# Performance work log

Measured on AMD Instinct MI355X. Metric: run time of the kernel, lower is better.

## Reference

```python
import jax, jax.numpy as jnp
import numpy as np

B, M, K, P = 64, 8, 4, 16  # batch, rx antennas, streams, constellation size
NBPS = 4  # 16-QAM


def _qam_points(nbps):
    # square QAM, unit average energy
    n = 2 ** (nbps // 2)
    pam = 2.0 * np.arange(n) - n + 1.0  # e.g. {-3,-1,1,3}
    re, im = np.meshgrid(pam, pam, indexing='ij')
    pts = (re + 1j * im).reshape(-1)
    pts = pts / np.sqrt(np.mean(np.abs(pts) ** 2))
    return pts.astype(np.complex64)


def _build_vecs(points, k):
    # replicate MaximumLikelihoodDetector._build_vecs: stream 0 varies slowest
    p = points.shape[0]
    grids = np.meshgrid(*([np.arange(p)] * k), indexing='ij')
    idx = np.stack(grids, axis=-1).reshape(-1, k)        # [P^K, K]
    vecs = points[idx]                                   # [P^K, K] complex
    c = np.stack([
        np.stack([np.where(idx[:, j] == pi)[0] for j in range(k)], axis=-1)
        for pi in range(p)
    ], axis=-1)                                          # [P^(K-1), K, P]
    return vecs, c.astype(np.int32)


def setup_inputs() -> dict:
    key = jax.random.key(0)
    ks = jax.random.split(key, 6)
    points = _qam_points(NBPS)
    vecs, c = _build_vecs(points, K)
    yr = jax.random.normal(ks[0], (B, M), jnp.float32)
    yi = jax.random.normal(ks[1], (B, M), jnp.float32)
    hr = jax.random.normal(ks[2], (B, M, K), jnp.float32)
    hi = jax.random.normal(ks[3], (B, M, K), jnp.float32)
    # Hermitian positive-definite noise covariance s = A A^H / M + I
    ar = jax.random.normal(ks[4], (B, M, M), jnp.float32)
    ai = jax.random.normal(ks[5], (B, M, M), jnp.float32)
    a = (ar + 1j * ai).astype(jnp.complex64)
    s = a @ jnp.conj(jnp.swapaxes(a, -1, -2)) / M + jnp.eye(M, dtype=jnp.complex64)
    return {
        'yr': yr, 'yi': yi, 'hr': hr, 'hi': hi,
        'sr': jnp.real(s).astype(jnp.float32), 'si': jnp.imag(s).astype(jnp.float32),
        'vr': jnp.asarray(vecs.real), 'vi': jnp.asarray(vecs.imag),
        'c': jnp.asarray(c),
    }


def reference(yr, yi, hr, hi, sr, si, vr, vi, c):
    y = (yr + 1j * yi).astype(jnp.complex64)          # [B, M]
    h = (hr + 1j * hi).astype(jnp.complex64)          # [B, M, K]
    s = (sr + 1j * si).astype(jnp.complex64)          # [B, M, M]
    vecs = (vr + 1j * vi).astype(jnp.complex64)       # [V, K]
    # whitening: s_inv = inv(cholesky(s))
    L = jnp.linalg.cholesky(s)
    s_inv = jnp.linalg.inv(L)                         # [B, M, M]
    yw = jnp.einsum('bmn,bn->bm', s_inv, y)           # [B, M]
    hw = jnp.einsum('bmn,bnk->bmk', s_inv, h)         # [B, M, K]
    # distances for every candidate symbol vector
    hv = jnp.einsum('bmk,vk->bvm', hw, vecs)          # [B, V, M]
    diff = yw[:, None, :] - hv                        # [B, V, M]
    exponents = -jnp.sum(diff.real ** 2 + diff.imag ** 2, axis=-1)  # [B, V]
    # regroup exponents by (stream, symbol) and reduce (app -> logsumexp)
    exp_g = exponents[:, c]                           # [B, P^(K-1), K, P]
    logits = jax.nn.logsumexp(exp_g, axis=-3)         # [B, K, P]
    return logits
```

## Files before the change

### kernel.cpp

```cpp
#include <hip/hip_runtime.h>
#include <math.h>


__global__ __launch_bounds__(256) void k_main(
    const float* __restrict__ yr, const float* __restrict__ yi,
    const float* __restrict__ hr, const float* __restrict__ hi,
    const float* __restrict__ sr, const float* __restrict__ si,
    const float* __restrict__ vr, const float* __restrict__ vi,
    float* __restrict__ ws, float* __restrict__ out)
{
    __shared__ float sL[8][8][2];
    __shared__ float sDinv[8];
    __shared__ float lyw[8][2];
    __shared__ float lhw[8][4][2];
    __shared__ float tab[4][8][16][2];
    __shared__ float pn2b[16];
    __shared__ float Hn1b;
    __shared__ float xbuf[16][256];
    __shared__ float pmax[256];
    __shared__ float cm[16][17];
    __shared__ float m1buf[16], m2buf[16], m3buf[16];
    __shared__ float part2[256], part3[256];
    __shared__ float s2buf[16];

    const int t = threadIdx.x;
    const int b = blockIdx.x >> 4, chunk = blockIdx.x & 15;
    const int lane = t & 63, wv = t >> 6;
    const int i3 = t & 15, i2 = t >> 4;

    if (wv == 0) {
        float ar_[8] = {}, ai_[8] = {}, Lr_[8] = {}, Li_[8] = {};
        if (lane < 8) {
#pragma unroll
            for (int k = 0; k < 8; ++k) {
                ar_[k] = sr[b * 64 + lane * 8 + k];
                ai_[k] = si[b * 64 + lane * 8 + k];
            }
        }
        float inv = 0.f;
#pragma unroll
        for (int j = 0; j < 8; ++j) {
            if (lane == j) {
                float d = ar_[j];
#pragma unroll
                for (int k = 0; k < 8; ++k) if (k < j) d -= Lr_[k]*Lr_[k] + Li_[k]*Li_[k];
                float ld = sqrtf(d);
                Lr_[j] = ld; Li_[j] = 0.f;
                inv = 1.f / ld;
                sDinv[j] = inv;
            }
            float invj = __shfl(inv, j);
            float cr = ar_[j], ci = ai_[j];
#pragma unroll
            for (int k = 0; k < 8; ++k) if (k < j) {
                float Ljrk = __shfl(Lr_[k], j);
                float Ljik = __shfl(Li_[k], j);
                cr -= Lr_[k]*Ljrk + Li_[k]*Ljik;
                ci -= Li_[k]*Ljrk - Lr_[k]*Ljik;
            }
            if (lane < 8 && lane > j) { Lr_[j] = cr * invj; Li_[j] = ci * invj; }
        }
        if (lane < 8) {
#pragma unroll
            for (int k = 0; k < 8; ++k) if (k <= lane) { sL[lane][k][0] = Lr_[k]; sL[lane][k][1] = Li_[k]; }
        }
        if (lane < 5) {
            float rr[8], ri[8], zr[8], zi[8];
            if (lane == 0) {
#pragma unroll
                for (int i = 0; i < 8; ++i) { rr[i] = yr[b*8+i]; ri[i] = yi[b*8+i]; }
            } else {
#pragma unroll
                for (int i = 0; i < 8; ++i) { rr[i] = hr[(b*8+i)*4 + (lane-1)]; ri[i] = hi[(b*8+i)*4 + (lane-1)]; }
            }
#pragma unroll
            for (int i = 0; i < 8; ++i) {
                float cr = rr[i], ci = ri[i];
#pragma unroll
                for (int k = 0; k < 8; ++k) if (k < i) {
                    cr -= sL[i][k][0]*zr[k] - sL[i][k][1]*zi[k];
                    ci -= sL[i][k][0]*zi[k] + sL[i][k][1]*zr[k];
                }
                float dv = sDinv[i];
                zr[i] = cr * dv; zi[i] = ci * dv;
                if (lane == 0) { lyw[i][0] = zr[i]; lyw[i][1] = zi[i]; }
                else           { lhw[i][lane-1][0] = zr[i]; lhw[i][lane-1][1] = zi[i]; }
            }
        }
        {
            int p = lane & 15;
            float pr  = vr[(p << 12) * 4];
            float pim = vi[(p << 12) * 4];
            if (lane < 16) pn2b[lane] = pr*pr + pim*pim;
            if (lane == 0) {
                float hn = 0.f;
#pragma unroll
                for (int m = 0; m < 8; ++m) hn += lhw[m][1][0]*lhw[m][1][0] + lhw[m][1][1]*lhw[m][1][1];
                Hn1b = hn;
            }
#pragma unroll
            for (int it = 0; it < 8; ++it) {
                int e = lane + it * 64;
                int k = e >> 7, m = (e >> 4) & 7;
                float hre = lhw[m][k][0], him = lhw[m][k][1];
                tab[k][m][p][0] = hre*pr  - him*pim;
                tab[k][m][p][1] = hre*pim + him*pr;
            }
        }
    }
    __syncthreads();

    float br_[8], bi_[8];
    float B2 = 0.f;
#pragma unroll
    for (int m = 0; m < 8; ++m) {
        const float2 t0 = *(const float2*)&tab[0][m][chunk][0];
        const float2 t2 = *(const float2*)&tab[2][m][i2][0];
        const float2 t3 = *(const float2*)&tab[3][m][i3][0];
        const float2 yw = *(const float2*)&lyw[m][0];
        br_[m] = t0.x + t2.x + t3.x - yw.x;
        bi_[m] = t0.y + t2.y + t3.y - yw.y;
        B2 = fmaf(br_[m], br_[m], fmaf(bi_[m], bi_[m], B2));
    }
    const float Hn1 = Hn1b;

    float x_[16];
    float vmA = -3.4e38f;
#pragma unroll
    for (int s = 0; s < 16; ++s) {
        float D = 0.f;
#pragma unroll
        for (int m = 0; m < 8; ++m) {
            const float2 t1 = *(const float2*)&tab[1][m][s][0];
            D = fmaf(br_[m], t1.x, D);
            D = fmaf(bi_[m], t1.y, D);
        }
        float x = fmaf(-2.f, D, -fmaf(pn2b[s], Hn1, B2));
        x_[s] = x;
        vmA = fmaxf(vmA, x);
        xbuf[s][t] = x;
    }
    pmax[t] = vmA;
    __syncthreads();

    const int su = i3, seg = i2;
    {
        float m = -3.4e38f;
#pragma unroll
        for (int j = 0; j < 16; ++j) m = fmaxf(m, xbuf[su][seg*16 + ((j + su) & 15)]);
        cm[su][seg] = m;
    }
    if (t < 16) {
        float m = -3.4e38f;
#pragma unroll
        for (int j = 0; j < 16; ++j) m = fmaxf(m, pmax[t*16 + j]);
        m2buf[t] = m;
    } else if (t < 32) {
        int d = t - 16;
        float m = -3.4e38f;
#pragma unroll
        for (int j = 0; j < 16; ++j) m = fmaxf(m, pmax[d + 16*j]);
        m3buf[d] = m;
    }
    __syncthreads();

    if (t < 16) {
        float m = -3.4e38f;
#pragma unroll
        for (int j = 0; j < 16; ++j) m = fmaxf(m, cm[t][j]);
        m1buf[t] = m;
    }
    const float M2 = m2buf[i2], M3 = m3buf[i3];
    const float Mlo = fminf(M2, M3);
    float acc = 0.f;
#pragma unroll
    for (int s = 0; s < 16; ++s) acc += __expf(x_[s] - Mlo);
    part2[t] = acc * __expf(Mlo - M2);
    part3[t] = acc * __expf(Mlo - M3);
    __syncthreads();

    {
        const float M1 = m1buf[su];
        float ssum = 0.f;
#pragma unroll
        for (int j = 0; j < 16; ++j)
            ssum += __expf(xbuf[su][seg*16 + ((j + su) & 15)] - M1);
        cm[su][seg] = ssum;
    }
    if (t < 16) {
        float S2 = 0.f;
#pragma unroll
        for (int j = 0; j < 16; ++j) S2 += part2[t*16 + j];
        s2buf[t] = S2;
        float* w = ws + ((b*48 + 16 + t)*16 + chunk)*2;
        w[0] = m2buf[t]; w[1] = S2;
    } else if (t < 32) {
        int d = t - 16;
        float S3 = 0.f;
#pragma unroll
        for (int j = 0; j < 16; ++j) S3 += part3[d + 16*j];
        float* w = ws + ((b*48 + 32 + d)*16 + chunk)*2;
        w[0] = m3buf[d]; w[1] = S3;
    }
    __syncthreads();

    if (t < 16) {
        float S1 = 0.f;
#pragma unroll
        for (int j = 0; j < 16; ++j) S1 += cm[t][j];
        float* w = ws + ((b*48 + t)*16 + chunk)*2;
        w[0] = m1buf[t]; w[1] = S1;
    }
    if (t == 16) {
        float M0 = m2buf[0];
#pragma unroll
        for (int i = 1; i < 16; ++i) M0 = fmaxf(M0, m2buf[i]);
        float S0 = 0.f;
#pragma unroll
        for (int i = 0; i < 16; ++i) S0 += s2buf[i] * __expf(m2buf[i] - M0);
        out[b*64 + chunk] = __logf(S0) + M0;
    }
}

__global__ __launch_bounds__(256) void k_comb(const float* __restrict__ ws, float* __restrict__ out)
{
    int idx = blockIdx.x * 256 + threadIdx.x;
    if (idx >= 64 * 48) return;
    int b = idx / 48, gi = idx % 48;
    const float* p = ws + (b*48 + gi)*32;
    float M = p[0];
#pragma unroll
    for (int i = 1; i < 16; ++i) M = fmaxf(M, p[2*i]);
    float S = 0.f;
#pragma unroll
    for (int i = 0; i < 16; ++i) S += p[2*i+1] * __expf(p[2*i] - M);
    out[b*64 + 16 + gi] = __logf(S) + M;
}

extern "C" void kernel_launch(void* const* d_in, const int* in_sizes, int n_in,
                              void* d_out, int out_size, void* d_ws, size_t ws_size,
                              hipStream_t stream) {
    const float* yr = (const float*)d_in[0];
    const float* yi = (const float*)d_in[1];
    const float* hr = (const float*)d_in[2];
    const float* hi = (const float*)d_in[3];
    const float* sr = (const float*)d_in[4];
    const float* si = (const float*)d_in[5];
    const float* vr = (const float*)d_in[6];
    const float* vi = (const float*)d_in[7];
    float* ws = (float*)d_ws;
    float* out = (float*)d_out;
    hipLaunchKernelGGL(k_main, dim3(1024), dim3(256), 0, stream,
                       yr, yi, hr, hi, sr, si, vr, vi, ws, out);
    hipLaunchKernelGGL(k_comb, dim3(12), dim3(256), 0, stream, ws, out);
}
```

Before: 19.71 us.

## Fuse into one per-batch kernel using Gram-matrix expansion of distances

Replaces the two-kernel design (1024 blocks plus a combine kernel) with one 1024-thread block per batch element that loops over 16 chunks and combines the logsumexp pairs in shared memory. Distances are expanded algebraically into precomputed Gram terms (per-stream norms, pairwise cross terms, projections onto yw), so each candidate costs a few table adds instead of an 8-element complex dot product. It also switches to exp2/log2 hardware builtins with pre-scaled constants and staggers the shared-memory reduction reads. This removes the second launch and the workspace round trip, at the cost of far fewer blocks (64) and more block-wide barriers per block.

```diff
diff --git a/kernel.cpp b/kernel.cpp
--- a/kernel.cpp
+++ b/kernel.cpp
@@ -1,34 +1,55 @@
 #include <hip/hip_runtime.h>
 #include <math.h>
 
-
-__global__ __launch_bounds__(256) void k_main(
+#define LOG2E 1.4426950408889634f
+#define LN2   0.6931471805599453f
+
+#if __has_builtin(__builtin_amdgcn_exp2f)
+#define EXP2(x) __builtin_amdgcn_exp2f(x)
+#else
+#define EXP2(x) exp2f(x)
+#endif
+#if __has_builtin(__builtin_amdgcn_logf)
+#define LOG2(x) __builtin_amdgcn_logf(x)
+#else
+#define LOG2(x) log2f(x)
+#endif
+
+
+__global__ __launch_bounds__(1024) void k_all(
     const float* __restrict__ yr, const float* __restrict__ yi,
     const float* __restrict__ hr, const float* __restrict__ hi,
     const float* __restrict__ sr, const float* __restrict__ si,
     const float* __restrict__ vr, const float* __restrict__ vi,
-    float* __restrict__ ws, float* __restrict__ out)
+    float* __restrict__ out)
 {
     __shared__ float sL[8][8][2];
     __shared__ float sDinv[8];
     __shared__ float lyw[8][2];
     __shared__ float lhw[8][4][2];
-    __shared__ float tab[4][8][16][2];
-    __shared__ float pn2b[16];
-    __shared__ float Hn1b;
-    __shared__ float xbuf[16][256];
-    __shared__ float pmax[256];
-    __shared__ float cm[16][17];
-    __shared__ float m1buf[16], m2buf[16], m3buf[16];
-    __shared__ float part2[256], part3[256];
-    __shared__ float s2buf[16];
+    __shared__ float ptr_[16], pti_[16];
+    __shared__ float gdiag[4];
+    __shared__ float gr2[6], gi2[6];
+    __shared__ float wr_[4], wi_[4];
+    __shared__ float u2s;
+    __shared__ float G2[4][16];
+    __shared__ float P2[6][16][16];
+    __shared__ float xbuf[4][16][256];
+    __shared__ float pmax[4][256];
+    __shared__ float cm[4][16][17];
+    __shared__ float m1b[4][16], m2b[4][16], m3b[4][16], s2b[4][16];
+    __shared__ float part2[4][256], part3[4][256];
+    __shared__ float pairs[48][17][2];
 
     const int t = threadIdx.x;
-    const int b = blockIdx.x >> 4, chunk = blockIdx.x & 15;
-    const int lane = t & 63, wv = t >> 6;
-    const int i3 = t & 15, i2 = t >> 4;
-
-    if (wv == 0) {
+    const int b = blockIdx.x;
+    const int u = t >> 8, c = t & 255;
+    const int i2 = c >> 4, i3 = c & 15;
+
+    if (t < 16) { ptr_[t] = vr[(t << 12) * 4]; pti_[t] = vi[(t << 12) * 4]; }
+
+    if (t < 64) {
+        const int lane = t;
         float ar_[8] = {}, ai_[8] = {}, Lr_[8] = {}, Li_[8] = {};
         if (lane < 8) {
 #pragma unroll
@@ -87,154 +108,175 @@
                 else           { lhw[i][lane-1][0] = zr[i]; lhw[i][lane-1][1] = zi[i]; }
             }
         }
+    }
+    __syncthreads();
+
+    if (t < 15) {
+        if (t < 4) {
+            float s = 0.f;
+#pragma unroll
+            for (int m = 0; m < 8; ++m) {
+                float ar = lhw[m][t][0], ai = lhw[m][t][1];
+                s = fmaf(ar, ar, fmaf(ai, ai, s));
+            }
+            gdiag[t] = s;
+        } else if (t < 10) {
+            const int pi = t - 4;
+            const int pa_tab[6] = {0, 0, 0, 1, 1, 2};
+            const int pb_tab[6] = {1, 2, 3, 2, 3, 3};
+            const int pa = pa_tab[pi];
+            const int pb = pb_tab[pi];
+            float srr = 0.f, sii = 0.f;
+#pragma unroll
+            for (int m = 0; m < 8; ++m) {
+                float ar = lhw[m][pa][0], ai = lhw[m][pa][1];
+                float br = lhw[m][pb][0], bi = lhw[m][pb][1];
+                srr = fmaf(ar, br, fmaf(ai, bi, srr));
+                sii = fmaf(ar, bi, fmaf(-ai, br, sii));
+            }
+            gr2[pi] = srr; gi2[pi] = sii;
+        } else if (t < 14) {
+            const int a = t - 10;
+            float swr = 0.f, swi = 0.f;
+#pragma unroll
+            for (int m = 0; m < 8; ++m) {
+                float ar = lhw[m][a][0], ai = lhw[m][a][1];
+                swr = fmaf(ar, lyw[m][0], fmaf(ai, lyw[m][1], swr));
+                swi = fmaf(ar, lyw[m][1], fmaf(-ai, lyw[m][0], swi));
+            }
+            wr_[a] = swr; wi_[a] = swi;
+        } else {
+            float s = 0.f;
+#pragma unroll
+            for (int m = 0; m < 8; ++m)
+                s = fmaf(lyw[m][0], lyw[m][0], fmaf(lyw[m][1], lyw[m][1], s));
+            u2s = LOG2E * s;
+        }
+    }
+    __syncthreads();
+
+    if (t < 64) {
+        const int a = t >> 4, v = t & 15;
+        float pn2 = ptr_[v]*ptr_[v] + pti_[v]*pti_[v];
+        G2[a][v] = LOG2E * (pn2 * gdiag[a] - 2.f*(ptr_[v]*wr_[a] + pti_[v]*wi_[a]));
+    }
+    for (int e = t; e < 1536; e += 1024) {
+        const int tb = e >> 8, va = (e >> 4) & 15, vb = e & 15;
+        float dotr = ptr_[va]*ptr_[vb] + pti_[va]*pti_[vb];
+        float doti = ptr_[va]*pti_[vb] - pti_[va]*ptr_[vb];
+        P2[tb][va][vb] = 2.f * LOG2E * (dotr*gr2[tb] - doti*gi2[tb]);
+    }
+    __syncthreads();
+
+    const float Kpart = u2s + G2[2][i2] + G2[3][i3] + P2[5][i2][i3];
+    float Rp[16];
+#pragma unroll
+    for (int s = 0; s < 16; ++s)
+        Rp[s] = G2[1][s] + P2[3][s][i2] + P2[4][s][i3];
+
+    for (int it = 0; it < 4; ++it) {
+        const int ch = u * 4 + it;
+        const float Kit = Kpart + G2[0][ch] + P2[1][ch][i2] + P2[2][ch][i3];
+        float xl[16];
+        float vmA = -3.4e38f;
+#pragma unroll
+        for (int s = 0; s < 16; ++s) {
+            float x = -(Kit + Rp[s] + P2[0][ch][s]);
+            xl[s] = x;
+            vmA = fmaxf(vmA, x);
+            xbuf[u][s][c] = x;
+        }
+        pmax[u][c] = vmA;
+        __syncthreads();
+
         {
-            int p = lane & 15;
-            float pr  = vr[(p << 12) * 4];
-            float pim = vi[(p << 12) * 4];
-            if (lane < 16) pn2b[lane] = pr*pr + pim*pim;
-            if (lane == 0) {
-                float hn = 0.f;
-#pragma unroll
-                for (int m = 0; m < 8; ++m) hn += lhw[m][1][0]*lhw[m][1][0] + lhw[m][1][1]*lhw[m][1][1];
-                Hn1b = hn;
-            }
-#pragma unroll
-            for (int it = 0; it < 8; ++it) {
-                int e = lane + it * 64;
-                int k = e >> 7, m = (e >> 4) & 7;
-                float hre = lhw[m][k][0], him = lhw[m][k][1];
-                tab[k][m][p][0] = hre*pr  - him*pim;
-                tab[k][m][p][1] = hre*pim + him*pr;
-            }
-        }
-    }
-    __syncthreads();
-
-    float br_[8], bi_[8];
-    float B2 = 0.f;
-#pragma unroll
-    for (int m = 0; m < 8; ++m) {
-        const float2 t0 = *(const float2*)&tab[0][m][chunk][0];
-        const float2 t2 = *(const float2*)&tab[2][m][i2][0];
-        const float2 t3 = *(const float2*)&tab[3][m][i3][0];
-        const float2 yw = *(const float2*)&lyw[m][0];
-        br_[m] = t0.x + t2.x + t3.x - yw.x;
-        bi_[m] = t0.y + t2.y + t3.y - yw.y;
-        B2 = fmaf(br_[m], br_[m], fmaf(bi_[m], bi_[m], B2));
-    }
-    const float Hn1 = Hn1b;
-
-    float x_[16];
-    float vmA = -3.4e38f;
-#pragma unroll
-    for (int s = 0; s < 16; ++s) {
-        float D = 0.f;
-#pragma unroll
-        for (int m = 0; m < 8; ++m) {
-            const float2 t1 = *(const float2*)&tab[1][m][s][0];
-            D = fmaf(br_[m], t1.x, D);
-            D = fmaf(bi_[m], t1.y, D);
-        }
-        float x = fmaf(-2.f, D, -fmaf(pn2b[s], Hn1, B2));
-        x_[s] = x;
-        vmA = fmaxf(vmA, x);
-        xbuf[s][t] = x;
-    }
-    pmax[t] = vmA;
-    __syncthreads();
-
-    const int su = i3, seg = i2;
-    {
-        float m = -3.4e38f;
-#pragma unroll
-        for (int j = 0; j < 16; ++j) m = fmaxf(m, xbuf[su][seg*16 + ((j + su) & 15)]);
-        cm[su][seg] = m;
-    }
-    if (t < 16) {
-        float m = -3.4e38f;
-#pragma unroll
-        for (int j = 0; j < 16; ++j) m = fmaxf(m, pmax[t*16 + j]);
-        m2buf[t] = m;
-    } else if (t < 32) {
-        int d = t - 16;
-        float m = -3.4e38f;
-#pragma unroll
-        for (int j = 0; j < 16; ++j) m = fmaxf(m, pmax[d + 16*j]);
-        m3buf[d] = m;
-    }
-    __syncthreads();
-
-    if (t < 16) {
-        float m = -3.4e38f;
-#pragma unroll
-        for (int j = 0; j < 16; ++j) m = fmaxf(m, cm[t][j]);
-        m1buf[t] = m;
-    }
-    const float M2 = m2buf[i2], M3 = m3buf[i3];
-    const float Mlo = fminf(M2, M3);
-    float acc = 0.f;
-#pragma unroll
-    for (int s = 0; s < 16; ++s) acc += __expf(x_[s] - Mlo);
-    part2[t] = acc * __expf(Mlo - M2);
-    part3[t] = acc * __expf(Mlo - M3);
-    __syncthreads();
-
-    {
-        const float M1 = m1buf[su];
-        float ssum = 0.f;
-#pragma unroll
-        for (int j = 0; j < 16; ++j)
-            ssum += __expf(xbuf[su][seg*16 + ((j + su) & 15)] - M1);
-        cm[su][seg] = ssum;
-    }
-    if (t < 16) {
-        float S2 = 0.f;
-#pragma unroll
-        for (int j = 0; j < 16; ++j) S2 += part2[t*16 + j];
-        s2buf[t] = S2;
-        float* w = ws + ((b*48 + 16 + t)*16 + chunk)*2;
-        w[0] = m2buf[t]; w[1] = S2;
-    } else if (t < 32) {
-        int d = t - 16;
-        float S3 = 0.f;
-#pragma unroll
-        for (int j = 0; j < 16; ++j) S3 += part3[d + 16*j];
-        float* w = ws + ((b*48 + 32 + d)*16 + chunk)*2;
-        w[0] = m3buf[d]; w[1] = S3;
-    }
-    __syncthreads();
-
-    if (t < 16) {
-        float S1 = 0.f;
-#pragma unroll
-        for (int j = 0; j < 16; ++j) S1 += cm[t][j];
-        float* w = ws + ((b*48 + t)*16 + chunk)*2;
-        w[0] = m1buf[t]; w[1] = S1;
-    }
-    if (t == 16) {
-        float M0 = m2buf[0];
-#pragma unroll
-        for (int i = 1; i < 16; ++i) M0 = fmaxf(M0, m2buf[i]);
-        float S0 = 0.f;
-#pragma unroll
-        for (int i = 0; i < 16; ++i) S0 += s2buf[i] * __expf(m2buf[i] - M0);
-        out[b*64 + chunk] = __logf(S0) + M0;
-    }
-}
-
-__global__ __launch_bounds__(256) void k_comb(const float* __restrict__ ws, float* __restrict__ out)
-{
-    int idx = blockIdx.x * 256 + threadIdx.x;
-    if (idx >= 64 * 48) return;
-    int b = idx / 48, gi = idx % 48;
-    const float* p = ws + (b*48 + gi)*32;
-    float M = p[0];
-#pragma unroll
-    for (int i = 1; i < 16; ++i) M = fmaxf(M, p[2*i]);
-    float S = 0.f;
-#pragma unroll
-    for (int i = 0; i < 16; ++i) S += p[2*i+1] * __expf(p[2*i] - M);
-    out[b*64 + 16 + gi] = __logf(S) + M;
+            float m = -3.4e38f;
+#pragma unroll
+            for (int j = 0; j < 16; ++j) m = fmaxf(m, xbuf[u][i3][i2*16 + ((j + i3) & 15)]);
+            cm[u][i3][i2] = m;
+        }
+        if (c < 16) {
+            float m = -3.4e38f;
+#pragma unroll
+            for (int j = 0; j < 16; ++j) m = fmaxf(m, pmax[u][c*16 + ((j + c) & 15)]);
+            m2b[u][c] = m;
+        } else if (c < 32) {
+            const int d = c - 16;
+            float m = -3.4e38f;
+#pragma unroll
+            for (int j = 0; j < 16; ++j) m = fmaxf(m, pmax[u][d + 16*((j + d) & 15)]);
+            m3b[u][d] = m;
+        }
+        __syncthreads();
+
+        if (c < 16) {
+            float m = -3.4e38f;
+#pragma unroll
+            for (int j = 0; j < 16; ++j) m = fmaxf(m, cm[u][c][j]);
+            m1b[u][c] = m;
+        }
+        const float M2 = m2b[u][i2], M3 = m3b[u][i3];
+        const float Mlo = fminf(M2, M3);
+        float acc = 0.f;
+#pragma unroll
+        for (int s = 0; s < 16; ++s) acc += EXP2(xl[s] - Mlo);
+        part2[u][c] = acc * EXP2(Mlo - M2);
+        part3[u][c] = acc * EXP2(Mlo - M3);
+        __syncthreads();
+
+        {
+            const float M1 = m1b[u][i3];
+            float ssum = 0.f;
+#pragma unroll
+            for (int j = 0; j < 16; ++j)
+                ssum += EXP2(xbuf[u][i3][i2*16 + ((j + i3) & 15)] - M1);
+            cm[u][i3][i2] = ssum;
+        }
+        if (c < 16) {
+            float S2 = 0.f;
+#pragma unroll
+            for (int j = 0; j < 16; ++j) S2 += part2[u][c*16 + ((j + c) & 15)];
+            s2b[u][c] = S2;
+            pairs[16 + c][ch][0] = m2b[u][c];
+            pairs[16 + c][ch][1] = S2;
+        } else if (c < 32) {
+            const int d = c - 16;
+            float S3 = 0.f;
+#pragma unroll
+            for (int j = 0; j < 16; ++j) S3 += part3[u][d + 16*((j + d) & 15)];
+            pairs[32 + d][ch][0] = m3b[u][d];
+            pairs[32 + d][ch][1] = S3;
+        }
+        __syncthreads();
+
+        if (c < 16) {
+            float S1 = 0.f;
+#pragma unroll
+            for (int j = 0; j < 16; ++j) S1 += cm[u][c][j];
+            pairs[c][ch][0] = m1b[u][c];
+            pairs[c][ch][1] = S1;
+        }
+        if (c == 16) {
+            float M0 = m2b[u][0];
+#pragma unroll
+            for (int i = 1; i < 16; ++i) M0 = fmaxf(M0, m2b[u][i]);
+            float S0 = 0.f;
+#pragma unroll
+            for (int i = 0; i < 16; ++i) S0 += s2b[u][i] * EXP2(m2b[u][i] - M0);
+            out[b*64 + ch] = LN2 * (LOG2(S0) + M0);
+        }
+        __syncthreads();
+    }
+
+    if (t < 48) {
+        float M = pairs[t][0][0];
+#pragma unroll
+        for (int i = 1; i < 16; ++i) M = fmaxf(M, pairs[t][i][0]);
+        float S = 0.f;
+#pragma unroll
+        for (int i = 0; i < 16; ++i) S += pairs[t][i][1] * EXP2(pairs[t][i][0] - M);
+        out[b*64 + 16 + t] = LN2 * (LOG2(S) + M);
+    }
 }
 
 extern "C" void kernel_launch(void* const* d_in, const int* in_sizes, int n_in,
@@ -248,9 +290,7 @@
     const float* si = (const float*)d_in[5];
     const float* vr = (const float*)d_in[6];
     const float* vi = (const float*)d_in[7];
-    float* ws = (float*)d_ws;
     float* out = (float*)d_out;
-    hipLaunchKernelGGL(k_main, dim3(1024), dim3(256), 0, stream,
-                       yr, yi, hr, hi, sr, si, vr, vi, ws, out);
-    hipLaunchKernelGGL(k_comb, dim3(12), dim3(256), 0, stream, ws, out);
+    hipLaunchKernelGGL(k_all, dim3(64), dim3(1024), 0, stream,
+                       yr, yi, hr, hi, sr, si, vr, vi, out);
 }
```

Result: slower. 36.14 us (+83.4%).
